# Optimization experiments

Measured on AMD Instinct MI355X. Metric: run time of the kernel, lower is better.

Reference implementation:

```python
import jax, jax.numpy as jnp
import numpy as np
import math

D = 1024
H = 16

def _new_gelu(x):
    return 0.5 * x * (1.0 + jnp.tanh(math.sqrt(2.0 / math.pi) * (x + 0.044715 * x ** 3)))

def _layer_norm(x, w):
    mu = jnp.mean(x, axis=-1, keepdims=True)
    var = jnp.var(x, axis=-1, keepdims=True)
    return (x - mu) * jax.lax.rsqrt(var + 1e-5) * w

def setup_inputs() -> dict:
    key = jax.random.key(0)
    ks = jax.random.split(key, 8)
    B, T = 2, 2048
    s = lambda fan_in: 1.0 / math.sqrt(fan_in)
    return {
        "x": jax.random.normal(ks[0], (B, T, D), jnp.float32),
        "ln1_w": jnp.ones((D,), jnp.float32),
        "attn_w": jax.random.normal(ks[1], (D, 3 * D), jnp.float32) * s(D),
        "attn_b": jnp.zeros((3 * D,), jnp.float32),
        "proj_w": jax.random.normal(ks[2], (D, D), jnp.float32) * s(D),
        "proj_b": jnp.zeros((D,), jnp.float32),
        "ln2_w": jnp.ones((D,), jnp.float32),
        "li1_w": jax.random.normal(ks[3], (D, 4 * D), jnp.float32) * s(D),
        "li1_b": jnp.zeros((4 * D,), jnp.float32),
        "li2_w": jax.random.normal(ks[4], (4 * D, D), jnp.float32) * s(4 * D),
        "li2_b": jnp.zeros((D,), jnp.float32),
    }

def reference(x, ln1_w, attn_w, attn_b, proj_w, proj_b, ln2_w, li1_w, li1_b, li2_w, li2_b):
    B, T, C = x.shape
    Dh = C // H
    # --- causal self-attention on pre-LN input ---
    h = _layer_norm(x, ln1_w)
    qkv = h @ attn_w + attn_b                      # [B,T,3C]
    q, k, v = jnp.split(qkv, 3, axis=-1)
    q = q.reshape(B, T, H, Dh)
    k = k.reshape(B, T, H, Dh)
    v = v.reshape(B, T, H, Dh)
    # NOTE: faithful to source — scale is 1/sqrt(BATCH), not 1/sqrt(head_dim)
    scale = 1.0 / math.sqrt(B)
    scores = jnp.einsum('bthd,bshd->bhts', q, k) * scale   # [B,H,T,T]
    causal = jnp.tril(jnp.ones((T, T), bool))
    scores = jnp.where(causal, scores, -jnp.inf)
    attn = jax.nn.softmax(scores, axis=-1)
    o = jnp.einsum('bhts,bshd->bthd', attn, v).reshape(B, T, C)
    x = x + o @ proj_w + proj_b
    # --- MLP ---
    h = _layer_norm(x, ln2_w)
    x = x + _new_gelu(h @ li1_w + li1_b) @ li2_w + li2_b
    return x
```

## Files before the change

### kernel.cpp

```cpp
#include <hip/hip_runtime.h>

typedef _Float16 f16;
typedef _Float16 f16x8 __attribute__((ext_vector_type(8)));
typedef _Float16 f16x4 __attribute__((ext_vector_type(4)));
typedef float    f32x4 __attribute__((ext_vector_type(4)));
typedef float    f32x16 __attribute__((ext_vector_type(16)));
typedef unsigned u32;
typedef unsigned u32x4 __attribute__((ext_vector_type(4)));

#define GAS __attribute__((address_space(1)))
#define LAS __attribute__((address_space(3)))

static __device__ __forceinline__ void gload_lds16(const void* g, void* l) {
    __builtin_amdgcn_global_load_lds((const GAS void*)g, (LAS void*)l, 16, 0, 0);
}

__global__ void wconv_t(const float* __restrict__ w, f16* __restrict__ wt, int K, int N) {
    __shared__ f16 t[32][33];
    const int tx = threadIdx.x, ty = threadIdx.y;
    const int n0 = blockIdx.x * 32, k0 = blockIdx.y * 32;
#pragma unroll
    for (int i = 0; i < 4; i++)
        t[ty + i * 8][tx] = (f16)w[(size_t)(k0 + ty + i * 8) * N + n0 + tx];
    __syncthreads();
#pragma unroll
    for (int i = 0; i < 4; i++)
        wt[(size_t)(n0 + ty + i * 8) * K + k0 + tx] = t[tx][ty + i * 8];
}

__global__ __launch_bounds__(256) void ln_kernel(const float* __restrict__ x,
                                                 const float* __restrict__ w,
                                                 f16* __restrict__ h) {
    const int row = blockIdx.x, tid = threadIdx.x;
    const float4 v = reinterpret_cast<const float4*>(x)[(size_t)row * 256 + tid];
    float s = v.x + v.y + v.z + v.w;
    float q = v.x * v.x + v.y * v.y + v.z * v.z + v.w * v.w;
#pragma unroll
    for (int m = 1; m < 64; m <<= 1) { s += __shfl_xor(s, m); q += __shfl_xor(q, m); }
    __shared__ float ss[4], qq[4];
    if ((tid & 63) == 0) { ss[tid >> 6] = s; qq[tid >> 6] = q; }
    __syncthreads();
    s = ss[0] + ss[1] + ss[2] + ss[3];
    q = qq[0] + qq[1] + qq[2] + qq[3];
    const float mu = s * (1.0f / 1024.0f);
    const float var = q * (1.0f / 1024.0f) - mu * mu;
    const float rs = rsqrtf(var + 1e-5f);
    const float4 wv = reinterpret_cast<const float4*>(w)[tid];
    f16x4 o;
    o[0] = (f16)((v.x - mu) * rs * wv.x);
    o[1] = (f16)((v.y - mu) * rs * wv.y);
    o[2] = (f16)((v.z - mu) * rs * wv.z);
    o[3] = (f16)((v.w - mu) * rs * wv.w);
    reinterpret_cast<f16x4*>(h)[(size_t)row * 256 + tid] = o;
}

__global__ __launch_bounds__(256) void vtrans(const f16* __restrict__ V, f16* __restrict__ Vt) {
    __shared__ f16 tl[64][72];
    const int tid = threadIdx.x;
    const int t0 = blockIdx.x * 64, bh = blockIdx.y;
    const int b = bh >> 4, hh = bh & 15;
    const int rr = tid >> 3, cc = (tid & 7) * 8;
#pragma unroll
    for (int p = 0; p < 2; p++) {
        f16x8 v = *(const f16x8*)(V + (size_t)(b * 2048 + t0 + p * 32 + rr) * 1024 + hh * 64 + cc);
#pragma unroll
        for (int j = 0; j < 8; j++) tl[p * 32 + rr][cc + j] = v[j];
    }
    __syncthreads();
#pragma unroll
    for (int p = 0; p < 2; p++) {
        const int d = p * 32 + rr;
        f16x8 o;
#pragma unroll
        for (int j = 0; j < 8; j++) o[j] = tl[cc + j][d];
        *(f16x8*)(Vt + (size_t)(bh * 64 + d) * 2048 + t0 + cc) = o;
    }
}

template <int EPI>
__global__ __launch_bounds__(512) void gemm_f16(
    const f16* __restrict__ A, int lda,
    const f16* __restrict__ Bt, int ldb,
    const float* __restrict__ bias,
    const float* __restrict__ res,
    void* __restrict__ outp,
    f16* __restrict__ oq, f16* __restrict__ ok, f16* __restrict__ ov,
    int N, int K) {
    __shared__ alignas(16) f16 As[3][128 * 32];
    __shared__ alignas(16) f16 Bs[3][128 * 32];
    const int tid = threadIdx.x;
    const int lane = tid & 63, wv = tid >> 6;
    const int wr = wv >> 2, wc = wv & 3;
    const int m0 = blockIdx.x * 128, n0 = blockIdx.y * 128;
    const int l15 = lane & 15, lg = lane >> 4;

    f32x4 acc[4][2] = {};

    const int ar = tid >> 2;
    const int ac = (tid & 3) * 8;
    const size_t koff = (size_t)blockIdx.z * K;
    const f16* gA = A + (size_t)(m0 + ar) * lda + ac + koff;
    const f16* gB = Bt + (size_t)(n0 + ar) * ldb + ac + koff;
    char* lA0 = (char*)As + wv * 1024;
    char* lB0 = (char*)Bs + wv * 1024;

    auto stage = [&](int buf, int k0) {
        gload_lds16(gA + k0, lA0 + buf * 8192);
        gload_lds16(gB + k0, lB0 + buf * 8192);
    };
    auto compute = [&](int buf) {
        f16x8 af[4], bf[2];
#pragma unroll
        for (int i = 0; i < 4; i++)
            af[i] = *(const f16x8*)&As[buf][(wr * 64 + i * 16 + l15) * 32 + lg * 8];
#pragma unroll
        for (int n = 0; n < 2; n++)
            bf[n] = *(const f16x8*)&Bs[buf][(wc * 32 + n * 16 + l15) * 32 + lg * 8];
#pragma unroll
        for (int mi = 0; mi < 4; mi++)
#pragma unroll
            for (int ni = 0; ni < 2; ni++)
                acc[mi][ni] = __builtin_amdgcn_mfma_f32_16x16x32_f16(af[mi], bf[ni], acc[mi][ni], 0, 0, 0);
    };

    const int nk = K >> 5;
    stage(0, 0);
    if (nk > 1) {
        stage(1, 32);
        asm volatile("s_waitcnt vmcnt(2)" ::: "memory");
    } else {
        asm volatile("s_waitcnt vmcnt(0)" ::: "memory");
    }
    __builtin_amdgcn_s_barrier();

    for (int t = 0; t < nk; ++t) {
        const bool pref = (t + 2 < nk);
        if (pref) stage((t + 2) % 3, (t + 2) * 32);
        compute(t % 3);
        if (t + 1 < nk) {
            if (pref) asm volatile("s_waitcnt vmcnt(2)" ::: "memory");
            else      asm volatile("s_waitcnt vmcnt(0)" ::: "memory");
            __builtin_amdgcn_s_barrier();
        }
    }

#pragma unroll
    for (int mi = 0; mi < 4; mi++) {
#pragma unroll
        for (int ni = 0; ni < 2; ni++) {
            const int gc = n0 + wc * 32 + ni * 16 + l15;
            const float bb = (EPI == 3) ? 0.0f : bias[gc];
#pragma unroll
            for (int r = 0; r < 4; r++) {
                const int gr = m0 + wr * 64 + mi * 16 + lg * 4 + r;
                float v = acc[mi][ni][r] + bb;
                if (EPI == 0) {
                    if (gc < 1024)      oq[(size_t)gr * 1024 + gc]        = (f16)(v * 0.70710678118654752f);
                    else if (gc < 2048) ok[(size_t)gr * 1024 + gc - 1024] = (f16)v;
                    else                ov[(size_t)gr * 1024 + gc - 2048] = (f16)v;
                } else if (EPI == 1) {
                    ((float*)outp)[(size_t)gr * N + gc] = v + res[(size_t)gr * N + gc];
                } else if (EPI == 2) {
                    const float z = 0.7978845608028654f * (v + 0.044715f * v * v * v);
                    const float t = 1.0f - 2.0f / (__builtin_amdgcn_exp2f(2.8853900817779268f * z) + 1.0f);
                    ((f16*)outp)[(size_t)gr * N + gc] = (f16)(0.5f * v * (1.0f + t));
                } else {
                    float* P = (float*)outp + (size_t)blockIdx.z * ((size_t)gridDim.x * 128) * N;
                    P[(size_t)gr * N + gc] = v;
                }
            }
        }
    }
}

__global__ __launch_bounds__(256) void kred(const float* __restrict__ p0,
                                            const float* __restrict__ p1,
                                            const float* __restrict__ bias,
                                            const float* __restrict__ res,
                                            float* __restrict__ out) {
    const size_t i = (size_t)blockIdx.x * 256 + threadIdx.x;
    const float4 a = ((const float4*)p0)[i];
    const float4 b = ((const float4*)p1)[i];
    const float4 r = ((const float4*)res)[i];
    const float4 w = ((const float4*)bias)[i & 255];
    float4 o;
    o.x = a.x + b.x + r.x + w.x;
    o.y = a.y + b.y + r.y + w.y;
    o.z = a.z + b.z + r.z + w.z;
    o.w = a.w + b.w + r.w + w.w;
    ((float4*)out)[i] = o;
}

__global__ __launch_bounds__(256) void attn_kernel(
    const f16* __restrict__ Q, const f16* __restrict__ Kb,
    const f16* __restrict__ Vt, f16* __restrict__ O) {
    __shared__ alignas(16) char pool[24576];
    const int tid = threadIdx.x, lane = tid & 63, w = tid >> 6;
    const int l31 = lane & 31, hi = lane >> 5;
    const int bx = blockIdx.x;
    const int j = bx >> 5, bh = bx & 31;
    const int qb = (j < 8) ? (15 - 2 * j) : (2 * (j - 8));
    const int b = bh >> 4, hh = bh & 15;
    const int qtile = qb * 4 + w;
    const int q0 = qtile * 32;
    const int ntw = qtile + 1;
    const int nk = qb * 4 + 4;

    const f16* qrow = Q + (size_t)(b * 2048 + q0 + l31) * 1024 + hh * 64 + hi * 8;
    f16x8 qf[4];
#pragma unroll
    for (int s = 0; s < 4; s++) qf[s] = *(const f16x8*)(qrow + s * 16);

    f32x16 oacc[2] = {};
    float m = -3e38f, l = 0.0f;

    const f16* kg = Kb + (size_t)b * 2048 * 1024 + (size_t)(tid >> 3) * 1024 + hh * 64
                    + ((tid & 7) ^ ((tid >> 3) & 7)) * 8;
    const f16* vg = Vt + (size_t)(bh * 64 + (tid >> 2)) * 2048
                    + (((tid & 3) ^ ((tid >> 3) & 3)) * 8);
    char* kld = pool + tid * 16;
    char* vld = pool + 4096 + tid * 16;

    auto stage = [&](int buf, int kt) {
        gload_lds16(kg + (size_t)kt * 32768, kld + buf * 8192);
        gload_lds16(vg + kt * 32, vld + buf * 8192);
    };

    const int ksw = (l31 & 7);
    const int vsw = ((l31 >> 1) & 3);

    auto tilestep = [&](int buf, bool diag) {
        const f16* Kbuf = (const f16*)(pool + buf * 8192);
        const f16* Vbuf = (const f16*)(pool + buf * 8192 + 4096);
        f16x8 kf[4], vf[4];
#pragma unroll
        for (int si = 0; si < 4; si++)
            kf[si] = *(const f16x8*)&Kbuf[l31 * 64 + (((si * 2 + hi) ^ ksw) * 8)];
        vf[0] = *(const f16x8*)&Vbuf[l31 * 32 + ((hi ^ vsw) * 8)];
        vf[1] = *(const f16x8*)&Vbuf[l31 * 32 + (((2 + hi) ^ vsw) * 8)];
        vf[2] = *(const f16x8*)&Vbuf[(32 + l31) * 32 + ((hi ^ vsw) * 8)];
        vf[3] = *(const f16x8*)&Vbuf[(32 + l31) * 32 + (((2 + hi) ^ vsw) * 8)];

        f32x16 sacc = {};
        __builtin_amdgcn_s_setprio(1);
#pragma unroll
        for (int s = 0; s < 4; s++)
            sacc = __builtin_amdgcn_mfma_f32_32x32x16_f16(kf[s], qf[s], sacc, 0, 0, 0);
        __builtin_amdgcn_s_setprio(0);
        if (diag) {
#pragma unroll
            for (int r = 0; r < 16; r++) {
                const int key = (r & 3) + 8 * (r >> 2) + 4 * hi;
                sacc[r] = (key > l31) ? -3e38f : sacc[r];
            }
        }
        float t8[8];
#pragma unroll
        for (int i = 0; i < 8; i++) t8[i] = fmaxf(sacc[2 * i], sacc[2 * i + 1]);
#pragma unroll
        for (int i = 0; i < 4; i++) t8[i] = fmaxf(t8[i], t8[i + 4]);
        float tm = fmaxf(fmaxf(t8[0], t8[1]), fmaxf(t8[2], t8[3]));
        tm = fmaxf(tm, __shfl_xor(tm, 32));
        const bool up = tm > m + 8.0f;
        if (__any(up)) {
            const float mnew = up ? tm : m;
            const float alpha = __expf(m - mnew);
            m = mnew;
            l *= alpha;
#pragma unroll
            for (int r = 0; r < 16; r++) { oacc[0][r] *= alpha; oacc[1][r] *= alpha; }
        }
        const float mref = m * 1.44269504f;
        float p[16];
#pragma unroll
        for (int r = 0; r < 16; r++)
            p[r] = __builtin_amdgcn_exp2f(sacc[r] * 1.44269504f - mref);
        float s8[8];
#pragma unroll
        for (int i = 0; i < 8; i++) s8[i] = p[2 * i] + p[2 * i + 1];
#pragma unroll
        for (int i = 0; i < 4; i++) s8[i] = s8[i] + s8[i + 4];
        float psum = (s8[0] + s8[1]) + (s8[2] + s8[3]);
        psum += __shfl_xor(psum, 32);
        l += psum;

        u32 wd[8];
#pragma unroll
        for (int i = 0; i < 8; i++)
            wd[i] = __builtin_bit_cast(u32, __builtin_amdgcn_cvt_pkrtz(p[2 * i], p[2 * i + 1]));
        const u32 e0 = __shfl_xor(hi ? wd[0] : wd[2], 32);
        const u32 e1 = __shfl_xor(hi ? wd[1] : wd[3], 32);
        const u32 e2 = __shfl_xor(hi ? wd[4] : wd[6], 32);
        const u32 e3 = __shfl_xor(hi ? wd[5] : wd[7], 32);
        u32x4 b0, b1;
        b0[0] = hi ? e0 : wd[0]; b0[1] = hi ? e1 : wd[1];
        b0[2] = hi ? wd[2] : e0; b0[3] = hi ? wd[3] : e1;
        b1[0] = hi ? e2 : wd[4]; b1[1] = hi ? e3 : wd[5];
        b1[2] = hi ? wd[6] : e2; b1[3] = hi ? wd[7] : e3;
        const f16x8 pb0 = __builtin_bit_cast(f16x8, b0);
        const f16x8 pb1 = __builtin_bit_cast(f16x8, b1);

        __builtin_amdgcn_s_setprio(1);
        oacc[0] = __builtin_amdgcn_mfma_f32_32x32x16_f16(vf[0], pb0, oacc[0], 0, 0, 0);
        oacc[0] = __builtin_amdgcn_mfma_f32_32x32x16_f16(vf[1], pb1, oacc[0], 0, 0, 0);
        oacc[1] = __builtin_amdgcn_mfma_f32_32x32x16_f16(vf[2], pb0, oacc[1], 0, 0, 0);
        oacc[1] = __builtin_amdgcn_mfma_f32_32x32x16_f16(vf[3], pb1, oacc[1], 0, 0, 0);
        __builtin_amdgcn_s_setprio(0);
    };

    stage(0, 0);
    stage(1, 1);
    asm volatile("s_waitcnt vmcnt(2)" ::: "memory");
    __builtin_amdgcn_s_barrier();
    for (int t = 0; t < nk; ++t) {
        const bool pref = (t + 2 < nk);
        if (pref) stage((t + 2) % 3, t + 2);
        if (t < ntw) tilestep(t % 3, t == qtile);
        if (t + 1 < nk) {
            if (pref) asm volatile("s_waitcnt vmcnt(2)" ::: "memory");
            else      asm volatile("s_waitcnt vmcnt(0)" ::: "memory");
            __builtin_amdgcn_s_barrier();
        }
    }

    __syncthreads();
    f16* otw = (f16*)(pool) + w * (32 * 72);
    const float inv = 1.0f / l;
#pragma unroll
    for (int dt = 0; dt < 2; dt++)
#pragma unroll
        for (int r = 0; r < 16; r++) {
            const int d = dt * 32 + (r & 3) + 8 * (r >> 2) + 4 * hi;
            otw[l31 * 72 + d] = (f16)(oacc[dt][r] * inv);
        }
    asm volatile("s_waitcnt lgkmcnt(0)" ::: "memory");
#pragma unroll
    for (int i = 0; i < 4; i++) {
        const int row = i * 8 + (lane >> 3), col = (lane & 7) * 8;
        const f16x8 o8 = *(const f16x8*)&otw[row * 72 + col];
        *(f16x8*)(O + (size_t)(b * 2048 + q0 + row) * 1024 + hh * 64 + col) = o8;
    }
}

extern "C" void kernel_launch(void* const* d_in, const int* in_sizes, int n_in,
                              void* d_out, int out_size, void* d_ws, size_t ws_size,
                              hipStream_t stream) {
    const float* x      = (const float*)d_in[0];
    const float* ln1_w  = (const float*)d_in[1];
    const float* attn_w = (const float*)d_in[2];
    const float* attn_b = (const float*)d_in[3];
    const float* proj_w = (const float*)d_in[4];
    const float* proj_b = (const float*)d_in[5];
    const float* ln2_w  = (const float*)d_in[6];
    const float* li1_w  = (const float*)d_in[7];
    const float* li1_b  = (const float*)d_in[8];
    const float* li2_w  = (const float*)d_in[9];
    const float* li2_b  = (const float*)d_in[10];
    float* out = (float*)d_out;

    char* ws = (char*)d_ws;
    size_t off = 0;
    auto alloc = [&](size_t bytes) { void* p = ws + off; off += (bytes + 255) & ~(size_t)255; return p; };
    f16* W1t = (f16*)alloc((size_t)3072 * 1024 * 2);
    f16* W2t = (f16*)alloc((size_t)1024 * 1024 * 2);
    f16* W3t = (f16*)alloc((size_t)4096 * 1024 * 2);
    f16* W4t = (f16*)alloc((size_t)1024 * 4096 * 2);
    f16* h   = (f16*)alloc((size_t)4096 * 1024 * 2);
    f16* Qb  = (f16*)alloc((size_t)4096 * 1024 * 2);
    f16* Kb  = (f16*)alloc((size_t)4096 * 1024 * 2);
    f16* Vb  = (f16*)alloc((size_t)4096 * 1024 * 2);
    f16* Vt  = (f16*)alloc((size_t)4096 * 1024 * 2);
    f16* Ob  = (f16*)alloc((size_t)4096 * 1024 * 2);
    float* x1 = (float*)alloc((size_t)4096 * 1024 * 4);
    float* P  = (float*)alloc((size_t)2 * 4096 * 1024 * 4);
    f16* Ab = Qb;

    dim3 b328(32, 8);
    wconv_t<<<dim3(96, 32),  b328, 0, stream>>>(attn_w, W1t, 1024, 3072);
    wconv_t<<<dim3(32, 32),  b328, 0, stream>>>(proj_w, W2t, 1024, 1024);
    wconv_t<<<dim3(128, 32), b328, 0, stream>>>(li1_w,  W3t, 1024, 4096);
    wconv_t<<<dim3(32, 128), b328, 0, stream>>>(li2_w,  W4t, 4096, 1024);

    ln_kernel<<<4096, 256, 0, stream>>>(x, ln1_w, h);
    gemm_f16<0><<<dim3(32, 24), 512, 0, stream>>>(h, 1024, W1t, 1024, attn_b, nullptr,
                                                  nullptr, Qb, Kb, Vb, 3072, 1024);
    vtrans<<<dim3(32, 32), 256, 0, stream>>>(Vb, Vt);
    attn_kernel<<<512, 256, 0, stream>>>(Qb, Kb, Vt, Ob);
    gemm_f16<1><<<dim3(32, 8), 512, 0, stream>>>(Ob, 1024, W2t, 1024, proj_b, x,
                                                 x1, nullptr, nullptr, nullptr, 1024, 1024);
    ln_kernel<<<4096, 256, 0, stream>>>(x1, ln2_w, h);
    gemm_f16<2><<<dim3(32, 32), 512, 0, stream>>>(h, 1024, W3t, 1024, li1_b, nullptr,
                                                  Ab, nullptr, nullptr, nullptr, 4096, 1024);
    gemm_f16<3><<<dim3(32, 8, 2), 512, 0, stream>>>(Ab, 4096, W4t, 4096, nullptr, nullptr,
                                                    P, nullptr, nullptr, nullptr, 1024, 2048);
    kred<<<4096, 256, 0, stream>>>(P, P + (size_t)4096 * 1024, li2_b, x1, out);
}
```

Baseline: 277.8 us.

## Restructure attention into 8-wave blocks with strided query tiles and 64-key tiles

```diff
diff --git a/kernel.cpp b/kernel.cpp
--- a/kernel.cpp
+++ b/kernel.cpp
@@ -191,20 +191,19 @@
     ((float4*)out)[i] = o;
 }
 
-__global__ __launch_bounds__(256) void attn_kernel(
+__global__ __launch_bounds__(512) void attn_kernel(
     const f16* __restrict__ Q, const f16* __restrict__ Kb,
     const f16* __restrict__ Vt, f16* __restrict__ O) {
-    __shared__ alignas(16) char pool[24576];
+    __shared__ alignas(16) char pool[32768];
     const int tid = threadIdx.x, lane = tid & 63, w = tid >> 6;
     const int l31 = lane & 31, hi = lane >> 5;
     const int bx = blockIdx.x;
-    const int j = bx >> 5, bh = bx & 31;
-    const int qb = (j < 8) ? (15 - 2 * j) : (2 * (j - 8));
+    const int qs = bx >> 5, bh = bx & 31;
     const int b = bh >> 4, hh = bh & 15;
-    const int qtile = qb * 4 + w;
+    const int qtile = w * 8 + qs;
     const int q0 = qtile * 32;
-    const int ntw = qtile + 1;
-    const int nk = qb * 4 + 4;
+    const int last = qtile >> 1;
+    const int nk = ((56 + qs) >> 1) + 1;
 
     const f16* qrow = Q + (size_t)(b * 2048 + q0 + l31) * 1024 + hh * 64 + hi * 8;
     f16x8 qf[4];
@@ -214,49 +213,66 @@
     f32x16 oacc[2] = {};
     float m = -3e38f, l = 0.0f;
 
-    const f16* kg = Kb + (size_t)b * 2048 * 1024 + (size_t)(tid >> 3) * 1024 + hh * 64
-                    + ((tid & 7) ^ ((tid >> 3) & 7)) * 8;
-    const f16* vg = Vt + (size_t)(bh * 64 + (tid >> 2)) * 2048
-                    + (((tid & 3) ^ ((tid >> 3) & 3)) * 8);
+    const int srow = tid >> 3, sslot = (tid & 7) ^ ((tid >> 3) & 7);
+    const f16* kg = Kb + ((size_t)b * 2048 + srow) * 1024 + hh * 64 + sslot * 8;
+    const f16* vg = Vt + ((size_t)bh * 64 + srow) * 2048 + sslot * 8;
     char* kld = pool + tid * 16;
-    char* vld = pool + 4096 + tid * 16;
+    char* vld = pool + 8192 + tid * 16;
 
     auto stage = [&](int buf, int kt) {
-        gload_lds16(kg + (size_t)kt * 32768, kld + buf * 8192);
-        gload_lds16(vg + kt * 32, vld + buf * 8192);
+        gload_lds16(kg + (size_t)kt * 65536, kld + buf * 16384);
+        gload_lds16(vg + kt * 64, vld + buf * 16384);
     };
 
-    const int ksw = (l31 & 7);
-    const int vsw = ((l31 >> 1) & 3);
+    const int rs = l31 & 7;
 
     auto tilestep = [&](int buf, bool diag) {
-        const f16* Kbuf = (const f16*)(pool + buf * 8192);
-        const f16* Vbuf = (const f16*)(pool + buf * 8192 + 4096);
-        f16x8 kf[4], vf[4];
-#pragma unroll
-        for (int si = 0; si < 4; si++)
-            kf[si] = *(const f16x8*)&Kbuf[l31 * 64 + (((si * 2 + hi) ^ ksw) * 8)];
-        vf[0] = *(const f16x8*)&Vbuf[l31 * 32 + ((hi ^ vsw) * 8)];
-        vf[1] = *(const f16x8*)&Vbuf[l31 * 32 + (((2 + hi) ^ vsw) * 8)];
-        vf[2] = *(const f16x8*)&Vbuf[(32 + l31) * 32 + ((hi ^ vsw) * 8)];
-        vf[3] = *(const f16x8*)&Vbuf[(32 + l31) * 32 + (((2 + hi) ^ vsw) * 8)];
-
-        f32x16 sacc = {};
+        const f16* Kbuf = (const f16*)(pool + buf * 16384);
+        const f16* Vbuf = (const f16*)(pool + buf * 16384 + 8192);
+        const bool doH1 = !diag || (qtile & 1);
+        const int triH = qtile & 1;
+
+        f16x8 k0[4], k1[4];
+#pragma unroll
+        for (int s = 0; s < 4; s++)
+            k0[s] = *(const f16x8*)&Kbuf[l31 * 64 + (((s * 2 + hi) ^ rs) * 8)];
+        if (doH1)
+#pragma unroll
+            for (int s = 0; s < 4; s++)
+                k1[s] = *(const f16x8*)&Kbuf[(32 + l31) * 64 + (((s * 2 + hi) ^ rs) * 8)];
+
+        f32x16 sacc0 = {}, sacc1 = {};
         __builtin_amdgcn_s_setprio(1);
 #pragma unroll
         for (int s = 0; s < 4; s++)
-            sacc = __builtin_amdgcn_mfma_f32_32x32x16_f16(kf[s], qf[s], sacc, 0, 0, 0);
+            sacc0 = __builtin_amdgcn_mfma_f32_32x32x16_f16(k0[s], qf[s], sacc0, 0, 0, 0);
+        if (doH1)
+#pragma unroll
+            for (int s = 0; s < 4; s++)
+                sacc1 = __builtin_amdgcn_mfma_f32_32x32x16_f16(k1[s], qf[s], sacc1, 0, 0, 0);
         __builtin_amdgcn_s_setprio(0);
+
         if (diag) {
-#pragma unroll
-            for (int r = 0; r < 16; r++) {
-                const int key = (r & 3) + 8 * (r >> 2) + 4 * hi;
-                sacc[r] = (key > l31) ? -3e38f : sacc[r];
+            if (triH == 0) {
+#pragma unroll
+                for (int r = 0; r < 16; r++) {
+                    const int keyoff = (r & 3) + 8 * (r >> 2) + 4 * hi;
+                    sacc0[r] = (keyoff > l31) ? -3e38f : sacc0[r];
+                }
+            } else {
+#pragma unroll
+                for (int r = 0; r < 16; r++) {
+                    const int keyoff = (r & 3) + 8 * (r >> 2) + 4 * hi;
+                    sacc1[r] = (keyoff > l31) ? -3e38f : sacc1[r];
+                }
             }
         }
         float t8[8];
 #pragma unroll
-        for (int i = 0; i < 8; i++) t8[i] = fmaxf(sacc[2 * i], sacc[2 * i + 1]);
+        for (int i = 0; i < 8; i++) t8[i] = fmaxf(sacc0[2 * i], sacc0[2 * i + 1]);
+        if (doH1)
+#pragma unroll
+            for (int i = 0; i < 8; i++) t8[i] = fmaxf(t8[i], fmaxf(sacc1[2 * i], sacc1[2 * i + 1]));
 #pragma unroll
         for (int i = 0; i < 4; i++) t8[i] = fmaxf(t8[i], t8[i + 4]);
         float tm = fmaxf(fmaxf(t8[0], t8[1]), fmaxf(t8[2], t8[3]));
@@ -271,74 +287,122 @@
             for (int r = 0; r < 16; r++) { oacc[0][r] *= alpha; oacc[1][r] *= alpha; }
         }
         const float mref = m * 1.44269504f;
-        float p[16];
-#pragma unroll
-        for (int r = 0; r < 16; r++)
-            p[r] = __builtin_amdgcn_exp2f(sacc[r] * 1.44269504f - mref);
-        float s8[8];
-#pragma unroll
-        for (int i = 0; i < 8; i++) s8[i] = p[2 * i] + p[2 * i + 1];
-#pragma unroll
-        for (int i = 0; i < 4; i++) s8[i] = s8[i] + s8[i + 4];
-        float psum = (s8[0] + s8[1]) + (s8[2] + s8[3]);
-        psum += __shfl_xor(psum, 32);
-        l += psum;
-
+
+        float psum = 0.0f;
         u32 wd[8];
-#pragma unroll
-        for (int i = 0; i < 8; i++)
-            wd[i] = __builtin_bit_cast(u32, __builtin_amdgcn_cvt_pkrtz(p[2 * i], p[2 * i + 1]));
+        {
+            float p[16];
+#pragma unroll
+            for (int r = 0; r < 16; r++)
+                p[r] = __builtin_amdgcn_exp2f(sacc0[r] * 1.44269504f - mref);
+            float s8[8];
+#pragma unroll
+            for (int i = 0; i < 8; i++) s8[i] = p[2 * i] + p[2 * i + 1];
+#pragma unroll
+            for (int i = 0; i < 4; i++) s8[i] = s8[i] + s8[i + 4];
+            psum += (s8[0] + s8[1]) + (s8[2] + s8[3]);
+#pragma unroll
+            for (int i = 0; i < 8; i++)
+                wd[i] = __builtin_bit_cast(u32, __builtin_amdgcn_cvt_pkrtz(p[2 * i], p[2 * i + 1]));
+        }
         const u32 e0 = __shfl_xor(hi ? wd[0] : wd[2], 32);
         const u32 e1 = __shfl_xor(hi ? wd[1] : wd[3], 32);
         const u32 e2 = __shfl_xor(hi ? wd[4] : wd[6], 32);
         const u32 e3 = __shfl_xor(hi ? wd[5] : wd[7], 32);
-        u32x4 b0, b1;
-        b0[0] = hi ? e0 : wd[0]; b0[1] = hi ? e1 : wd[1];
-        b0[2] = hi ? wd[2] : e0; b0[3] = hi ? wd[3] : e1;
-        b1[0] = hi ? e2 : wd[4]; b1[1] = hi ? e3 : wd[5];
-        b1[2] = hi ? wd[6] : e2; b1[3] = hi ? wd[7] : e3;
-        const f16x8 pb0 = __builtin_bit_cast(f16x8, b0);
-        const f16x8 pb1 = __builtin_bit_cast(f16x8, b1);
-
+        u32x4 c0, c1;
+        c0[0] = hi ? e0 : wd[0]; c0[1] = hi ? e1 : wd[1];
+        c0[2] = hi ? wd[2] : e0; c0[3] = hi ? wd[3] : e1;
+        c1[0] = hi ? e2 : wd[4]; c1[1] = hi ? e3 : wd[5];
+        c1[2] = hi ? wd[6] : e2; c1[3] = hi ? wd[7] : e3;
+        const f16x8 pb00 = __builtin_bit_cast(f16x8, c0);
+        const f16x8 pb01 = __builtin_bit_cast(f16x8, c1);
+
+        f16x8 vfa, vfb;
         __builtin_amdgcn_s_setprio(1);
-        oacc[0] = __builtin_amdgcn_mfma_f32_32x32x16_f16(vf[0], pb0, oacc[0], 0, 0, 0);
-        oacc[0] = __builtin_amdgcn_mfma_f32_32x32x16_f16(vf[1], pb1, oacc[0], 0, 0, 0);
-        oacc[1] = __builtin_amdgcn_mfma_f32_32x32x16_f16(vf[2], pb0, oacc[1], 0, 0, 0);
-        oacc[1] = __builtin_amdgcn_mfma_f32_32x32x16_f16(vf[3], pb1, oacc[1], 0, 0, 0);
+        vfa = *(const f16x8*)&Vbuf[l31 * 64 + ((hi ^ rs) * 8)];
+        vfb = *(const f16x8*)&Vbuf[l31 * 64 + (((2 + hi) ^ rs) * 8)];
+        oacc[0] = __builtin_amdgcn_mfma_f32_32x32x16_f16(vfa, pb00, oacc[0], 0, 0, 0);
+        oacc[0] = __builtin_amdgcn_mfma_f32_32x32x16_f16(vfb, pb01, oacc[0], 0, 0, 0);
+        vfa = *(const f16x8*)&Vbuf[(32 + l31) * 64 + ((hi ^ rs) * 8)];
+        vfb = *(const f16x8*)&Vbuf[(32 + l31) * 64 + (((2 + hi) ^ rs) * 8)];
+        oacc[1] = __builtin_amdgcn_mfma_f32_32x32x16_f16(vfa, pb00, oacc[1], 0, 0, 0);
+        oacc[1] = __builtin_amdgcn_mfma_f32_32x32x16_f16(vfb, pb01, oacc[1], 0, 0, 0);
         __builtin_amdgcn_s_setprio(0);
+
+        if (doH1) {
+            float p[16];
+#pragma unroll
+            for (int r = 0; r < 16; r++)
+                p[r] = __builtin_amdgcn_exp2f(sacc1[r] * 1.44269504f - mref);
+            float s8[8];
+#pragma unroll
+            for (int i = 0; i < 8; i++) s8[i] = p[2 * i] + p[2 * i + 1];
+#pragma unroll
+            for (int i = 0; i < 4; i++) s8[i] = s8[i] + s8[i + 4];
+            psum += (s8[0] + s8[1]) + (s8[2] + s8[3]);
+#pragma unroll
+            for (int i = 0; i < 8; i++)
+                wd[i] = __builtin_bit_cast(u32, __builtin_amdgcn_cvt_pkrtz(p[2 * i], p[2 * i + 1]));
+            const u32 f0 = __shfl_xor(hi ? wd[0] : wd[2], 32);
+            const u32 f1 = __shfl_xor(hi ? wd[1] : wd[3], 32);
+            const u32 f2 = __shfl_xor(hi ? wd[4] : wd[6], 32);
+            const u32 f3 = __shfl_xor(hi ? wd[5] : wd[7], 32);
+            u32x4 d0, d1;
+            d0[0] = hi ? f0 : wd[0]; d0[1] = hi ? f1 : wd[1];
+            d0[2] = hi ? wd[2] : f0; d0[3] = hi ? wd[3] : f1;
+            d1[0] = hi ? f2 : wd[4]; d1[1] = hi ? f3 : wd[5];
+            d1[2] = hi ? wd[6] : f2; d1[3] = hi ? wd[7] : f3;
+            const f16x8 pb10 = __builtin_bit_cast(f16x8, d0);
+            const f16x8 pb11 = __builtin_bit_cast(f16x8, d1);
+
+            __builtin_amdgcn_s_setprio(1);
+            vfa = *(const f16x8*)&Vbuf[l31 * 64 + (((4 + hi) ^ rs) * 8)];
+            vfb = *(const f16x8*)&Vbuf[l31 * 64 + (((6 + hi) ^ rs) * 8)];
+            oacc[0] = __builtin_amdgcn_mfma_f32_32x32x16_f16(vfa, pb10, oacc[0], 0, 0, 0);
+            oacc[0] = __builtin_amdgcn_mfma_f32_32x32x16_f16(vfb, pb11, oacc[0], 0, 0, 0);
+            vfa = *(const f16x8*)&Vbuf[(32 + l31) * 64 + (((4 + hi) ^ rs) * 8)];
+            vfb = *(const f16x8*)&Vbuf[(32 + l31) * 64 + (((6 + hi) ^ rs) * 8)];
+            oacc[1] = __builtin_amdgcn_mfma_f32_32x32x16_f16(vfa, pb10, oacc[1], 0, 0, 0);
+            oacc[1] = __builtin_amdgcn_mfma_f32_32x32x16_f16(vfb, pb11, oacc[1], 0, 0, 0);
+            __builtin_amdgcn_s_setprio(0);
+        }
+        psum += __shfl_xor(psum, 32);
+        l += psum;
     };
 
     stage(0, 0);
-    stage(1, 1);
-    asm volatile("s_waitcnt vmcnt(2)" ::: "memory");
+    asm volatile("s_waitcnt vmcnt(0)" ::: "memory");
     __builtin_amdgcn_s_barrier();
+    int buf = 0;
     for (int t = 0; t < nk; ++t) {
-        const bool pref = (t + 2 < nk);
-        if (pref) stage((t + 2) % 3, t + 2);
-        if (t < ntw) tilestep(t % 3, t == qtile);
-        if (t + 1 < nk) {
-            if (pref) asm volatile("s_waitcnt vmcnt(2)" ::: "memory");
-            else      asm volatile("s_waitcnt vmcnt(0)" ::: "memory");
-            __builtin_amdgcn_s_barrier();
-        }
-    }
-
-    __syncthreads();
-    f16* otw = (f16*)(pool) + w * (32 * 72);
+        if (t + 1 < nk) stage(buf ^ 1, t + 1);
+        if (t <= last) tilestep(buf, t == last);
+        asm volatile("s_waitcnt vmcnt(0)" ::: "memory");
+        __builtin_amdgcn_s_barrier();
+        buf ^= 1;
+    }
+
     const float inv = 1.0f / l;
-#pragma unroll
-    for (int dt = 0; dt < 2; dt++)
-#pragma unroll
-        for (int r = 0; r < 16; r++) {
-            const int d = dt * 32 + (r & 3) + 8 * (r >> 2) + 4 * hi;
-            otw[l31 * 72 + d] = (f16)(oacc[dt][r] * inv);
-        }
-    asm volatile("s_waitcnt lgkmcnt(0)" ::: "memory");
-#pragma unroll
-    for (int i = 0; i < 4; i++) {
-        const int row = i * 8 + (lane >> 3), col = (lane & 7) * 8;
-        const f16x8 o8 = *(const f16x8*)&otw[row * 72 + col];
-        *(f16x8*)(O + (size_t)(b * 2048 + q0 + row) * 1024 + hh * 64 + col) = o8;
+    f16* ot = (f16*)pool + (w & 3) * (32 * 72);
+#pragma unroll
+    for (int g = 0; g < 2; g++) {
+        if ((w >> 2) == g) {
+#pragma unroll
+            for (int dt = 0; dt < 2; dt++)
+#pragma unroll
+                for (int r = 0; r < 16; r++) {
+                    const int d = dt * 32 + (r & 3) + 8 * (r >> 2) + 4 * hi;
+                    ot[l31 * 72 + d] = (f16)(oacc[dt][r] * inv);
+                }
+            asm volatile("s_waitcnt lgkmcnt(0)" ::: "memory");
+#pragma unroll
+            for (int i = 0; i < 4; i++) {
+                const int row = i * 8 + (lane >> 3), col = (lane & 7) * 8;
+                const f16x8 o8 = *(const f16x8*)&ot[row * 72 + col];
+                *(f16x8*)(O + (size_t)(b * 2048 + q0 + row) * 1024 + hh * 64 + col) = o8;
+            }
+        }
+        __syncthreads();
     }
 }
 
@@ -385,7 +449,7 @@
     gemm_f16<0><<<dim3(32, 24), 512, 0, stream>>>(h, 1024, W1t, 1024, attn_b, nullptr,
                                                   nullptr, Qb, Kb, Vb, 3072, 1024);
     vtrans<<<dim3(32, 32), 256, 0, stream>>>(Vb, Vt);
-    attn_kernel<<<512, 256, 0, stream>>>(Qb, Kb, Vt, Ob);
+    attn_kernel<<<256, 512, 0, stream>>>(Qb, Kb, Vt, Ob);
     gemm_f16<1><<<dim3(32, 8), 512, 0, stream>>>(Ob, 1024, W2t, 1024, proj_b, x,
                                                  x1, nullptr, nullptr, nullptr, 1024, 1024);
     ln_kernel<<<4096, 256, 0, stream>>>(x1, ln2_w, h);
```

Measured after the change: 261.0 us. -6.0%, faster.
